# Optimization experiments

Measured on AMD Instinct MI355X. Metric: run time of the kernel, lower is better.

## Reference

```python
import jax, jax.numpy as jnp
import numpy as np

N = 100000
E = 1600000
EMB = 64
IN = 64
HID = 64
HEADS = 3
NEG_SLOPE = 0.2            # PyG GATConv default LeakyReLU slope
RRELU_SLOPE = (1.0 / 8.0 + 1.0 / 3.0) / 2.0  # torch.rrelu eval-mode slope


def setup_inputs() -> dict:
    key = jax.random.key(0)
    ks = jax.random.split(key, 16)
    d_in = IN + EMB
    inp = {
        "z": jax.random.normal(ks[0], (N, EMB), jnp.float32),
        "x": jax.random.normal(ks[1], (N, IN), jnp.float32),
        "edge_index": jax.random.randint(ks[2], (2, E), 0, N, jnp.int32),
        # gat1: (in+emb) -> hidden, 3 heads, concat=False
        "W1": jax.random.normal(ks[3], (d_in, HEADS * HID), jnp.float32) / np.sqrt(d_in),
        "att_src1": jax.random.normal(ks[4], (HEADS, HID), jnp.float32) / np.sqrt(HID),
        "att_dst1": jax.random.normal(ks[5], (HEADS, HID), jnp.float32) / np.sqrt(HID),
        "bias1": jnp.zeros((HID,), jnp.float32),
        # gat2: hidden -> hidden, 3 heads, concat=True
        "W2": jax.random.normal(ks[6], (HID, HEADS * HID), jnp.float32) / np.sqrt(HID),
        "att_src2": jax.random.normal(ks[7], (HEADS, HID), jnp.float32) / np.sqrt(HID),
        "att_dst2": jax.random.normal(ks[8], (HEADS, HID), jnp.float32) / np.sqrt(HID),
        "bias2": jnp.zeros((HEADS * HID,), jnp.float32),
        # final linear hidden*3 -> 1 (with bias)
        "lin_w": jax.random.normal(ks[9], (HEADS * HID, 1), jnp.float32) / np.sqrt(HEADS * HID),
        "lin_b": jnp.zeros((1,), jnp.float32),
    }
    return inp


def rrelu_eval(x):
    return jnp.where(x >= 0, x, x * RRELU_SLOPE)


def gat_conv(x, src, dst, W, a_src, a_dst, bias, concat):
    """PyG GATConv (shared src/dst projection, self-loops already appended)."""
    n = x.shape[0]
    H, C = a_src.shape
    xl = (x @ W).reshape(n, H, C)                       # [N, H, C]
    s = jnp.einsum('nhc,hc->nh', xl, a_src)             # alpha_src per node
    d = jnp.einsum('nhc,hc->nh', xl, a_dst)             # alpha_dst per node
    alpha = jax.nn.leaky_relu(s[src] + d[dst], NEG_SLOPE)  # [E', H]
    amax = jax.ops.segment_max(alpha, dst, num_segments=n)
    ex = jnp.exp(alpha - amax[dst])
    denom = jax.ops.segment_sum(ex, dst, num_segments=n)
    w = ex / (denom[dst] + 1e-16)                       # segment softmax
    out = jax.ops.segment_sum(xl[src] * w[:, :, None], dst, num_segments=n)  # [N,H,C]
    out = out.reshape(n, H * C) if concat else out.mean(axis=1)
    return out + bias


def reference(z, x, edge_index, W1, att_src1, att_dst1, bias1,
              W2, att_src2, att_dst2, bias2, lin_w, lin_b):
    n = x.shape[0]
    loops = jnp.arange(n, dtype=edge_index.dtype)
    src = jnp.concatenate([edge_index[0], loops])       # add self-loops (PyG default)
    dst = jnp.concatenate([edge_index[1], loops])
    h = jnp.concatenate([z, x], axis=1)
    h = rrelu_eval(gat_conv(h, src, dst, W1, att_src1, att_dst1, bias1, concat=False))
    h = rrelu_eval(gat_conv(h, src, dst, W2, att_src2, att_dst2, bias2, concat=True))
    return h @ lin_w + lin_b
```

## Files before the change

### kernel.cpp

```cpp
#include <hip/hip_runtime.h>
#include <cstdint>
#include <cstddef>

#define NEG_SLOPE 0.2f
#define RRELU_SLOPE 0.22916666666666666f

#define BSHIFT 6
#define BCAP 1536
#define MAXNB 1600

typedef _Float16 half4 __attribute__((ext_vector_type(4)));
typedef _Float16 half8 __attribute__((ext_vector_type(8)));
typedef float f32x4 __attribute__((ext_vector_type(4)));

__device__ __forceinline__ float wave_sum64(float v) {
#pragma unroll
  for (int o = 32; o > 0; o >>= 1) v += __shfl_xor(v, o, 64);
  return v;
}

__global__ __launch_bounds__(256) void bucketA(const int* __restrict__ src,
                                               const int* __restrict__ dst, int E, int NB,
                                               int* __restrict__ cursor,
                                               int* __restrict__ region) {
  __shared__ int hist[MAXNB];
  __shared__ int gbase[MAXNB];
  const int tid = threadIdx.x;
  const int chunk = (E + gridDim.x - 1) / gridDim.x;
  const int e0 = blockIdx.x * chunk;
  const int e1 = min(e0 + chunk, E);
  for (int b = tid; b < NB; b += 256) hist[b] = 0;
  __syncthreads();
  for (int i = e0 + tid; i < e1; i += 256) {
    atomicAdd(&hist[dst[i] >> BSHIFT], 1);
  }
  __syncthreads();
  for (int b = tid; b < NB; b += 256) {
    int c = hist[b];
    gbase[b] = (c > 0) ? atomicAdd(&cursor[b], c) : 0;
    hist[b] = 0;
  }
  __syncthreads();
  for (int i = e0 + tid; i < e1; i += 256) {
    int d = dst[i];
    int b = d >> BSHIFT;
    int idx = atomicAdd(&hist[b], 1) + gbase[b];
    if (idx < BCAP) region[b * BCAP + idx] = src[i] | ((d & 63) << 17);
  }
}

__global__ __launch_bounds__(256) void bucket_scan(const int* __restrict__ cursor, int NB,
                                                   int* __restrict__ colbase) {
  __shared__ int lds[256];
  const int tid = threadIdx.x;
  const int K = (NB + 255) / 256;
  int vals[8];
  int s = 0;
#pragma unroll
  for (int j = 0; j < 8; j++) {
    int b = tid * K + j;
    int v = (j < K && b < NB) ? (min(cursor[b], BCAP) + 64) : 0;
    vals[j] = v;
    s += v;
  }
  lds[tid] = s;
  __syncthreads();
  for (int o = 1; o < 256; o <<= 1) {
    int t = (tid >= o) ? lds[tid - o] : 0;
    __syncthreads();
    lds[tid] += t;
    __syncthreads();
  }
  int off = (tid > 0) ? lds[tid - 1] : 0;
#pragma unroll
  for (int j = 0; j < 8; j++) {
    int b = tid * K + j;
    if (j < K && b < NB) colbase[b] = off;
    off += vals[j];
  }
}

__global__ __launch_bounds__(256) void bucketB(const int* __restrict__ region,
                                               const int* __restrict__ cursor,
                                               const int* __restrict__ colbase, int NB,
                                               int* __restrict__ rp, int* __restrict__ col) {
  __shared__ int lcnt[64];
  __shared__ int loff[64];
  const int b = blockIdx.x;
  const int tid = threadIdx.x;
  const int cnt = min(cursor[b], BCAP);
  const int base = colbase[b];
  if (tid < 64) lcnt[tid] = 0;
  __syncthreads();
  const int* reg = region + (size_t)b * BCAP;
  for (int i = tid; i < cnt; i += 256) {
    atomicAdd(&lcnt[reg[i] >> 17], 1);
  }
  __syncthreads();
  if (tid < 64) {
    int v = lcnt[tid] + 1;
    int inc = v;
#pragma unroll
    for (int o = 1; o < 64; o <<= 1) {
      int t = __shfl_up(inc, o, 64);
      if (tid >= o) inc += t;
    }
    int excl = inc - v;
    loff[tid] = excl;
    int n = (b << BSHIFT) + tid;
    rp[n] = base + excl;
    col[base + excl] = n;
    lcnt[tid] = 1;
  }
  __syncthreads();
  for (int i = tid; i < cnt; i += 256) {
    int r = reg[i];
    int ld = r >> 17;
    int idx = atomicAdd(&lcnt[ld], 1);
    col[base + loff[ld] + idx] = r & 0x1FFFF;
  }
}

#define APAD 72
#define BTPAD 72

template <int KC>
__global__ __launch_bounds__(256, 4) void gemm_sd_kernel(
    const float* __restrict__ A0, const float* __restrict__ A1,
    const float* __restrict__ W, const float* __restrict__ asrc,
    const float* __restrict__ adst, _Float16* __restrict__ xlh,
    float* __restrict__ sdS, float* __restrict__ sdD, int N) {
  __shared__ _Float16 A16[64 * APAD];
  __shared__ _Float16 Bt[192 * BTPAD];
  const int tid = threadIdx.x;
  const int w = tid >> 6;
  const int lane = tid & 63;
  const int m = lane & 15;
  const int q = lane >> 4;
  const int m0 = blockIdx.x * 64;

  f32x4 acc[12];
#pragma unroll
  for (int t = 0; t < 12; t++) acc[t] = (f32x4)(0.f);

  for (int kc = 0; kc < KC; kc++) {
    const float* __restrict__ Ab = (KC == 2 && kc == 1) ? A1 : A0;
    if (kc > 0) __syncthreads();
#pragma unroll
    for (int i = 0; i < 4; i++) {
      int f = tid + 256 * i;
      int row = f >> 4;
      int c4 = f & 15;
      int gr = m0 + row;
      gr = (gr < N) ? gr : (N - 1);
      float4 v = *(const float4*)(Ab + (size_t)gr * 64 + c4 * 4);
      half4 hv;
      hv.x = (_Float16)v.x; hv.y = (_Float16)v.y;
      hv.z = (_Float16)v.z; hv.w = (_Float16)v.w;
      *(half4*)&A16[row * APAD + c4 * 4] = hv;
    }
#pragma unroll
    for (int i = 0; i < 6; i++) {
      int f = tid + 256 * i;
      int kg = f / 192;
      int c = f % 192;
      half8 hv;
#pragma unroll
      for (int j = 0; j < 8; j++) {
        hv[j] = (_Float16)W[(size_t)(kc * 64 + kg * 8 + j) * 192 + c];
      }
      *(half8*)&Bt[c * BTPAD + kg * 8] = hv;
    }
    __syncthreads();

#pragma unroll
    for (int t = 0; t < 2; t++) {
      half8 af = *(const half8*)&A16[(w * 16 + m) * APAD + t * 32 + q * 8];
#pragma unroll
      for (int ct = 0; ct < 12; ct++) {
        half8 bf = *(const half8*)&Bt[(ct * 16 + m) * BTPAD + t * 32 + q * 8];
        acc[ct] = __builtin_amdgcn_mfma_f32_16x16x32_f16(af, bf, acc[ct], 0, 0, 0);
      }
    }
  }

  float avs[12], avd[12];
#pragma unroll
  for (int ct = 0; ct < 12; ct++) {
    avs[ct] = asrc[ct * 16 + m];
    avd[ct] = adst[ct * 16 + m];
  }
#pragma unroll
  for (int r = 0; r < 4; r++) {
    const int gr = m0 + w * 16 + q * 4 + r;
    const bool ok = gr < N;
    if (ok) {
#pragma unroll
      for (int ct = 0; ct < 12; ct++) {
        xlh[(size_t)gr * 192 + ct * 16 + m] = (_Float16)acc[ct][r];
      }
    }
#pragma unroll
    for (int h = 0; h < 3; h++) {
      float ps = acc[h * 4 + 0][r] * avs[h * 4 + 0] + acc[h * 4 + 1][r] * avs[h * 4 + 1] +
                 acc[h * 4 + 2][r] * avs[h * 4 + 2] + acc[h * 4 + 3][r] * avs[h * 4 + 3];
      float pd = acc[h * 4 + 0][r] * avd[h * 4 + 0] + acc[h * 4 + 1][r] * avd[h * 4 + 1] +
                 acc[h * 4 + 2][r] * avd[h * 4 + 2] + acc[h * 4 + 3][r] * avd[h * 4 + 3];
#pragma unroll
      for (int o = 1; o < 16; o <<= 1) {
        ps += __shfl_xor(ps, o, 64);
        pd += __shfl_xor(pd, o, 64);
      }
      if (ok && m == 0) {
        sdS[(size_t)gr * 4 + h] = ps;
        sdD[(size_t)gr * 4 + h] = pd;
      }
    }
  }
}

template <int D>
__device__ __forceinline__ void gather_fma_d(const _Float16* __restrict__ xlh,
                                             const float4* __restrict__ eb, int t, int par,
                                             unsigned laneoff, int h, float* acc) {
  half8 xv[D];
#pragma unroll
  for (int u = 0; u < D; u++) {
    float4 rec = eb[2 * (t + u) + par];
    unsigned off = (unsigned)__float_as_int(rec.x) * 384u + laneoff;
    xv[u] = *(const half8*)((const char*)xlh + off);
  }
#pragma unroll
  for (int u = 0; u < D; u++) {
    float4 rec = eb[2 * (t + u) + par];
    float w = (h == 0) ? rec.y : ((h == 1) ? rec.z : rec.w);
#pragma unroll
    for (int k = 0; k < 8; k++) acc[k] += (float)xv[u][k] * w;
  }
}

template <int MODE>
__global__ __launch_bounds__(256) void agg_kernel(
    const _Float16* __restrict__ xlh, const float4* __restrict__ sdS,
    const float4* __restrict__ sdD, const int* __restrict__ rp,
    const int* __restrict__ col, const float* __restrict__ bias,
    const float* __restrict__ lw, const float* __restrict__ lb,
    float* __restrict__ out, int N) {
  __shared__ float4 ebuf[4][64];
  const int lane = threadIdx.x & 63;
  const int wv = threadIdx.x >> 6;
  const int n = blockIdx.x * 4 + wv;
  if (n >= N) return;
  const int beg = rp[n], end = rp[n + 1];
  const float4 dd = sdD[n];
  const int s = lane & 31;
  const int h = (s < 24) ? (s >> 3) : 0;
  const int g = s & 7;
  const int par = lane >> 5;
  const unsigned laneoff = (unsigned)(h * 128 + g * 16);

  float l0 = 0.f, l1 = 0.f, l2 = 0.f;
  float acc[8];
#pragma unroll
  for (int k = 0; k < 8; k++) acc[k] = 0.f;

  for (int j0 = beg; j0 < end; j0 += 64) {
    const int cntc = min(64, end - j0);
    const bool valid = lane < cntc;
    int srcv = valid ? col[j0 + lane] : 0;
    float4 s4 = sdS[srcv];
    float t0 = s4.x + dd.x, t1 = s4.y + dd.y, t2 = s4.z + dd.z;
    t0 = (t0 < 0.f) ? t0 * NEG_SLOPE : t0;
    t1 = (t1 < 0.f) ? t1 * NEG_SLOPE : t1;
    t2 = (t2 < 0.f) ? t2 * NEG_SLOPE : t2;
    float e0 = valid ? __expf(t0) : 0.f;
    float e1 = valid ? __expf(t1) : 0.f;
    float e2 = valid ? __expf(t2) : 0.f;
    l0 += e0; l1 += e1; l2 += e2;
    ebuf[wv][lane] = make_float4(__int_as_float(srcv), e0, e1, e2);
    const float4* eb = ebuf[wv];
    const int steps = (cntc + 1) >> 1;
    int t = 0;
    for (; t + 7 <= steps; t += 7) {
      gather_fma_d<7>(xlh, eb, t, par, laneoff, h, acc);
    }
    if (t + 4 <= steps) {
      gather_fma_d<4>(xlh, eb, t, par, laneoff, h, acc);
      t += 4;
    }
    if (t + 2 <= steps) {
      gather_fma_d<2>(xlh, eb, t, par, laneoff, h, acc);
      t += 2;
    }
    if (t < steps) {
      gather_fma_d<1>(xlh, eb, t, par, laneoff, h, acc);
    }
  }

#pragma unroll
  for (int k = 0; k < 8; k++) acc[k] += __shfl_xor(acc[k], 32, 64);
  l0 = wave_sum64(l0);
  l1 = wave_sum64(l1);
  l2 = wave_sum64(l2);
  const float invl = 1.0f / (((h == 0) ? l0 : ((h == 1) ? l1 : l2)) + 1e-16f);
  float v[8];
#pragma unroll
  for (int k = 0; k < 8; k++) v[k] = acc[k] * invl;

  if (MODE == 1) {
    float m[8];
#pragma unroll
    for (int k = 0; k < 8; k++) {
      float a0 = __shfl(v[k], g, 64);
      float a1 = __shfl(v[k], g + 8, 64);
      float a2 = __shfl(v[k], g + 16, 64);
      m[k] = (a0 + a1 + a2) * (1.f / 3.f);
    }
    if (lane < 8) {
      float4 b0 = *(const float4*)(bias + g * 8);
      float4 b1 = *(const float4*)(bias + g * 8 + 4);
      float4 r0, r1;
      r0.x = m[0] + b0.x; r0.y = m[1] + b0.y; r0.z = m[2] + b0.z; r0.w = m[3] + b0.w;
      r1.x = m[4] + b1.x; r1.y = m[5] + b1.y; r1.z = m[6] + b1.z; r1.w = m[7] + b1.w;
      r0.x = (r0.x < 0.f) ? r0.x * RRELU_SLOPE : r0.x;
      r0.y = (r0.y < 0.f) ? r0.y * RRELU_SLOPE : r0.y;
      r0.z = (r0.z < 0.f) ? r0.z * RRELU_SLOPE : r0.z;
      r0.w = (r0.w < 0.f) ? r0.w * RRELU_SLOPE : r0.w;
      r1.x = (r1.x < 0.f) ? r1.x * RRELU_SLOPE : r1.x;
      r1.y = (r1.y < 0.f) ? r1.y * RRELU_SLOPE : r1.y;
      r1.z = (r1.z < 0.f) ? r1.z * RRELU_SLOPE : r1.z;
      r1.w = (r1.w < 0.f) ? r1.w * RRELU_SLOPE : r1.w;
      *(float4*)(out + (size_t)n * 64 + g * 8) = r0;
      *(float4*)(out + (size_t)n * 64 + g * 8 + 4) = r1;
    }
  } else {
    float part = 0.f;
    if (lane < 24) {
      const int c0 = h * 64 + g * 8;
      float4 b0 = *(const float4*)(bias + c0);
      float4 b1 = *(const float4*)(bias + c0 + 4);
      float4 w0 = *(const float4*)(lw + c0);
      float4 w1 = *(const float4*)(lw + c0 + 4);
      float r;
      r = v[0] + b0.x; r = (r < 0.f) ? r * RRELU_SLOPE : r; part += r * w0.x;
      r = v[1] + b0.y; r = (r < 0.f) ? r * RRELU_SLOPE : r; part += r * w0.y;
      r = v[2] + b0.z; r = (r < 0.f) ? r * RRELU_SLOPE : r; part += r * w0.z;
      r = v[3] + b0.w; r = (r < 0.f) ? r * RRELU_SLOPE : r; part += r * w0.w;
      r = v[4] + b1.x; r = (r < 0.f) ? r * RRELU_SLOPE : r; part += r * w1.x;
      r = v[5] + b1.y; r = (r < 0.f) ? r * RRELU_SLOPE : r; part += r * w1.y;
      r = v[6] + b1.z; r = (r < 0.f) ? r * RRELU_SLOPE : r; part += r * w1.z;
      r = v[7] + b1.w; r = (r < 0.f) ? r * RRELU_SLOPE : r; part += r * w1.w;
    }
    part = wave_sum64(part);
    if (lane == 0) out[n] = part + lb[0];
  }
}

extern "C" void kernel_launch(void* const* d_in, const int* in_sizes, int n_in,
                              void* d_out, int out_size, void* d_ws, size_t ws_size,
                              hipStream_t stream) {
  const float* z   = (const float*)d_in[0];
  const float* x   = (const float*)d_in[1];
  const int*   ei  = (const int*)d_in[2];
  const float* W1  = (const float*)d_in[3];
  const float* as1 = (const float*)d_in[4];
  const float* ad1 = (const float*)d_in[5];
  const float* b1  = (const float*)d_in[6];
  const float* W2  = (const float*)d_in[7];
  const float* as2 = (const float*)d_in[8];
  const float* ad2 = (const float*)d_in[9];
  const float* b2  = (const float*)d_in[10];
  const float* lw  = (const float*)d_in[11];
  const float* lb  = (const float*)d_in[12];
  float* out = (float*)d_out;

  const int N = in_sizes[0] / 64;
  const int E = in_sizes[2] / 2;
  const int* srcA = ei;
  const int* dstA = ei + E;
  const int NB = (N + 63) >> BSHIFT;

  char* ws = (char*)d_ws;
  size_t off = 0;
  auto alloc = [&](size_t bytes) -> void* {
    void* p = ws + off;
    off = (off + bytes + 255) & ~(size_t)255;
    return p;
  };
  _Float16* xlh = (_Float16*)alloc((size_t)N * 192 * 2);
  float* h1  = (float*)alloc((size_t)N * 64 * 4);
  float* sdS = (float*)alloc((size_t)N * 4 * 4);
  float* sdD = (float*)alloc((size_t)N * 4 * 4);
  int* region  = (int*)alloc((size_t)NB * BCAP * 4);
  int* cursor  = (int*)alloc((size_t)NB * 4);
  int* colbase = (int*)alloc((size_t)NB * 4);
  int* rp      = (int*)alloc(((size_t)NB * 64 + 1) * 4);
  int* col     = (int*)alloc(((size_t)E + (size_t)NB * 64) * 4);
  if (off > ws_size) return;

  hipMemsetAsync(cursor, 0, (size_t)NB * 4, stream);
  bucketA<<<128, 256, 0, stream>>>(srcA, dstA, E, NB, cursor, region);
  bucket_scan<<<1, 256, 0, stream>>>(cursor, NB, colbase);
  bucketB<<<NB, 256, 0, stream>>>(region, cursor, colbase, NB, rp, col);

  dim3 gg((N + 63) / 64);
  gemm_sd_kernel<2><<<gg, 256, 0, stream>>>(z, x, W1, as1, ad1, xlh, sdS, sdD, N);
  agg_kernel<1><<<(N + 3) / 4, 256, 0, stream>>>(xlh, (const float4*)sdS, (const float4*)sdD,
                                                 rp, col, b1, nullptr, nullptr, h1, N);
  gemm_sd_kernel<1><<<gg, 256, 0, stream>>>(h1, nullptr, W2, as2, ad2, xlh, sdS, sdD, N);
  agg_kernel<2><<<(N + 3) / 4, 256, 0, stream>>>(xlh, (const float4*)sdS, (const float4*)sdD,
                                                 rp, col, b2, lw, lb, out, N);
}
```

Before: 427.5 us.

## Fuse edge bucketing into first GEMM launch, pre-transpose weights, persistent aggregation

Edge bucketing (bucketA) now runs inside the same launch as the first projection GEMM, with distinct block ranges doing each job so the two independent stages overlap and one launch disappears. The weights are converted to transposed fp16 once by a small kernel, so GEMM blocks load them as vector half8 reads instead of strided scalar float loads with conversion. The aggregation kernels become grid-stride loops over a capped grid, which cuts block scheduling overhead. The trade-offs are an extra small launch for the weight conversion, dynamic shared memory sized to the larger GEMM footprint, and the bucketing blocks possibly serialising behind GEMM blocks.

```diff
diff --git a/kernel.cpp b/kernel.cpp
--- a/kernel.cpp
+++ b/kernel.cpp
@@ -19,15 +19,27 @@
   return v;
 }
 
-__global__ __launch_bounds__(256) void bucketA(const int* __restrict__ src,
-                                               const int* __restrict__ dst, int E, int NB,
-                                               int* __restrict__ cursor,
-                                               int* __restrict__ region) {
-  __shared__ int hist[MAXNB];
-  __shared__ int gbase[MAXNB];
+__global__ __launch_bounds__(256) void wcvt_kernel(const float* __restrict__ W1,
+                                                   const float* __restrict__ W2,
+                                                   _Float16* __restrict__ Wt1,
+                                                   _Float16* __restrict__ Wt2) {
+  const int c = blockIdx.x;
+  for (int k = threadIdx.x; k < 128; k += 256)
+    Wt1[(size_t)c * 128 + k] = (_Float16)W1[(size_t)k * 192 + c];
+  for (int k = threadIdx.x; k < 64; k += 256)
+    Wt2[(size_t)c * 64 + k] = (_Float16)W2[(size_t)k * 192 + c];
+}
+
+__device__ __forceinline__ void bucketA_body(char* smem, int bid, int nblk,
+                                             const int* __restrict__ src,
+                                             const int* __restrict__ dst, int E, int NB,
+                                             int* __restrict__ cursor,
+                                             int* __restrict__ region) {
+  int* hist = (int*)smem;
+  int* gbase = hist + MAXNB;
   const int tid = threadIdx.x;
-  const int chunk = (E + gridDim.x - 1) / gridDim.x;
-  const int e0 = blockIdx.x * chunk;
+  const int chunk = (E + nblk - 1) / nblk;
+  const int e0 = bid * chunk;
   const int e1 = min(e0 + chunk, E);
   for (int b = tid; b < NB; b += 256) hist[b] = 0;
   __syncthreads();
@@ -123,21 +135,23 @@
 
 #define APAD 72
 #define BTPAD 72
+#define GEMM_LDS (64 * APAD * 2 + 192 * BTPAD * 2)
 
 template <int KC>
-__global__ __launch_bounds__(256, 4) void gemm_sd_kernel(
+__device__ __forceinline__ void gemm_body(char* smem, int bid,
     const float* __restrict__ A0, const float* __restrict__ A1,
-    const float* __restrict__ W, const float* __restrict__ asrc,
+    const _Float16* __restrict__ Wt, const float* __restrict__ asrc,
     const float* __restrict__ adst, _Float16* __restrict__ xlh,
     float* __restrict__ sdS, float* __restrict__ sdD, int N) {
-  __shared__ _Float16 A16[64 * APAD];
-  __shared__ _Float16 Bt[192 * BTPAD];
+  _Float16* A16 = (_Float16*)smem;
+  _Float16* Bt = A16 + 64 * APAD;
   const int tid = threadIdx.x;
   const int w = tid >> 6;
   const int lane = tid & 63;
   const int m = lane & 15;
   const int q = lane >> 4;
-  const int m0 = blockIdx.x * 64;
+  const int m0 = bid * 64;
+  const int KW = KC * 64;
 
   f32x4 acc[12];
 #pragma unroll
@@ -164,11 +178,7 @@
       int f = tid + 256 * i;
       int kg = f / 192;
       int c = f % 192;
-      half8 hv;
-#pragma unroll
-      for (int j = 0; j < 8; j++) {
-        hv[j] = (_Float16)W[(size_t)(kc * 64 + kg * 8 + j) * 192 + c];
-      }
+      half8 hv = *(const half8*)&Wt[(size_t)c * KW + kc * 64 + kg * 8];
       *(half8*)&Bt[c * BTPAD + kg * 8] = hv;
     }
     __syncthreads();
@@ -216,6 +226,22 @@
         sdD[(size_t)gr * 4 + h] = pd;
       }
     }
+  }
+}
+
+template <int KC>
+__global__ __launch_bounds__(256, 4) void gemm_bucketA_fused(
+    const float* __restrict__ A0, const float* __restrict__ A1,
+    const _Float16* __restrict__ Wt, const float* __restrict__ asrc,
+    const float* __restrict__ adst, _Float16* __restrict__ xlh,
+    float* __restrict__ sdS, float* __restrict__ sdD, int N,
+    const int* __restrict__ src, const int* __restrict__ dst, int E, int NB,
+    int* __restrict__ cursor, int* __restrict__ region, int NBA) {
+  extern __shared__ char smem[];
+  if ((int)blockIdx.x < NBA) {
+    bucketA_body(smem, blockIdx.x, NBA, src, dst, E, NB, cursor, region);
+  } else {
+    gemm_body<KC>(smem, blockIdx.x - NBA, A0, A1, Wt, asrc, adst, xlh, sdS, sdD, N);
   }
 }
 
@@ -249,110 +275,112 @@
   __shared__ float4 ebuf[4][64];
   const int lane = threadIdx.x & 63;
   const int wv = threadIdx.x >> 6;
-  const int n = blockIdx.x * 4 + wv;
-  if (n >= N) return;
-  const int beg = rp[n], end = rp[n + 1];
-  const float4 dd = sdD[n];
   const int s = lane & 31;
   const int h = (s < 24) ? (s >> 3) : 0;
   const int g = s & 7;
   const int par = lane >> 5;
   const unsigned laneoff = (unsigned)(h * 128 + g * 16);
-
-  float l0 = 0.f, l1 = 0.f, l2 = 0.f;
-  float acc[8];
-#pragma unroll
-  for (int k = 0; k < 8; k++) acc[k] = 0.f;
-
-  for (int j0 = beg; j0 < end; j0 += 64) {
-    const int cntc = min(64, end - j0);
-    const bool valid = lane < cntc;
-    int srcv = valid ? col[j0 + lane] : 0;
-    float4 s4 = sdS[srcv];
-    float t0 = s4.x + dd.x, t1 = s4.y + dd.y, t2 = s4.z + dd.z;
-    t0 = (t0 < 0.f) ? t0 * NEG_SLOPE : t0;
-    t1 = (t1 < 0.f) ? t1 * NEG_SLOPE : t1;
-    t2 = (t2 < 0.f) ? t2 * NEG_SLOPE : t2;
-    float e0 = valid ? __expf(t0) : 0.f;
-    float e1 = valid ? __expf(t1) : 0.f;
-    float e2 = valid ? __expf(t2) : 0.f;
-    l0 += e0; l1 += e1; l2 += e2;
-    ebuf[wv][lane] = make_float4(__int_as_float(srcv), e0, e1, e2);
-    const float4* eb = ebuf[wv];
-    const int steps = (cntc + 1) >> 1;
-    int t = 0;
-    for (; t + 7 <= steps; t += 7) {
-      gather_fma_d<7>(xlh, eb, t, par, laneoff, h, acc);
-    }
-    if (t + 4 <= steps) {
-      gather_fma_d<4>(xlh, eb, t, par, laneoff, h, acc);
-      t += 4;
-    }
-    if (t + 2 <= steps) {
-      gather_fma_d<2>(xlh, eb, t, par, laneoff, h, acc);
-      t += 2;
-    }
-    if (t < steps) {
-      gather_fma_d<1>(xlh, eb, t, par, laneoff, h, acc);
-    }
-  }
-
-#pragma unroll
-  for (int k = 0; k < 8; k++) acc[k] += __shfl_xor(acc[k], 32, 64);
-  l0 = wave_sum64(l0);
-  l1 = wave_sum64(l1);
-  l2 = wave_sum64(l2);
-  const float invl = 1.0f / (((h == 0) ? l0 : ((h == 1) ? l1 : l2)) + 1e-16f);
-  float v[8];
-#pragma unroll
-  for (int k = 0; k < 8; k++) v[k] = acc[k] * invl;
-
-  if (MODE == 1) {
-    float m[8];
-#pragma unroll
-    for (int k = 0; k < 8; k++) {
-      float a0 = __shfl(v[k], g, 64);
-      float a1 = __shfl(v[k], g + 8, 64);
-      float a2 = __shfl(v[k], g + 16, 64);
-      m[k] = (a0 + a1 + a2) * (1.f / 3.f);
-    }
-    if (lane < 8) {
-      float4 b0 = *(const float4*)(bias + g * 8);
-      float4 b1 = *(const float4*)(bias + g * 8 + 4);
-      float4 r0, r1;
-      r0.x = m[0] + b0.x; r0.y = m[1] + b0.y; r0.z = m[2] + b0.z; r0.w = m[3] + b0.w;
-      r1.x = m[4] + b1.x; r1.y = m[5] + b1.y; r1.z = m[6] + b1.z; r1.w = m[7] + b1.w;
-      r0.x = (r0.x < 0.f) ? r0.x * RRELU_SLOPE : r0.x;
-      r0.y = (r0.y < 0.f) ? r0.y * RRELU_SLOPE : r0.y;
-      r0.z = (r0.z < 0.f) ? r0.z * RRELU_SLOPE : r0.z;
-      r0.w = (r0.w < 0.f) ? r0.w * RRELU_SLOPE : r0.w;
-      r1.x = (r1.x < 0.f) ? r1.x * RRELU_SLOPE : r1.x;
-      r1.y = (r1.y < 0.f) ? r1.y * RRELU_SLOPE : r1.y;
-      r1.z = (r1.z < 0.f) ? r1.z * RRELU_SLOPE : r1.z;
-      r1.w = (r1.w < 0.f) ? r1.w * RRELU_SLOPE : r1.w;
-      *(float4*)(out + (size_t)n * 64 + g * 8) = r0;
-      *(float4*)(out + (size_t)n * 64 + g * 8 + 4) = r1;
-    }
-  } else {
-    float part = 0.f;
-    if (lane < 24) {
-      const int c0 = h * 64 + g * 8;
-      float4 b0 = *(const float4*)(bias + c0);
-      float4 b1 = *(const float4*)(bias + c0 + 4);
-      float4 w0 = *(const float4*)(lw + c0);
-      float4 w1 = *(const float4*)(lw + c0 + 4);
-      float r;
-      r = v[0] + b0.x; r = (r < 0.f) ? r * RRELU_SLOPE : r; part += r * w0.x;
-      r = v[1] + b0.y; r = (r < 0.f) ? r * RRELU_SLOPE : r; part += r * w0.y;
-      r = v[2] + b0.z; r = (r < 0.f) ? r * RRELU_SLOPE : r; part += r * w0.z;
-      r = v[3] + b0.w; r = (r < 0.f) ? r * RRELU_SLOPE : r; part += r * w0.w;
-      r = v[4] + b1.x; r = (r < 0.f) ? r * RRELU_SLOPE : r; part += r * w1.x;
-      r = v[5] + b1.y; r = (r < 0.f) ? r * RRELU_SLOPE : r; part += r * w1.y;
-      r = v[6] + b1.z; r = (r < 0.f) ? r * RRELU_SLOPE : r; part += r * w1.z;
-      r = v[7] + b1.w; r = (r < 0.f) ? r * RRELU_SLOPE : r; part += r * w1.w;
-    }
-    part = wave_sum64(part);
-    if (lane == 0) out[n] = part + lb[0];
+  const int stride = gridDim.x * 4;
+
+  for (int n = blockIdx.x * 4 + wv; n < N; n += stride) {
+    const int beg = rp[n], end = rp[n + 1];
+    const float4 dd = sdD[n];
+
+    float l0 = 0.f, l1 = 0.f, l2 = 0.f;
+    float acc[8];
+#pragma unroll
+    for (int k = 0; k < 8; k++) acc[k] = 0.f;
+
+    for (int j0 = beg; j0 < end; j0 += 64) {
+      const int cntc = min(64, end - j0);
+      const bool valid = lane < cntc;
+      int srcv = valid ? col[j0 + lane] : 0;
+      float4 s4 = sdS[srcv];
+      float t0 = s4.x + dd.x, t1 = s4.y + dd.y, t2 = s4.z + dd.z;
+      t0 = (t0 < 0.f) ? t0 * NEG_SLOPE : t0;
+      t1 = (t1 < 0.f) ? t1 * NEG_SLOPE : t1;
+      t2 = (t2 < 0.f) ? t2 * NEG_SLOPE : t2;
+      float e0 = valid ? __expf(t0) : 0.f;
+      float e1 = valid ? __expf(t1) : 0.f;
+      float e2 = valid ? __expf(t2) : 0.f;
+      l0 += e0; l1 += e1; l2 += e2;
+      ebuf[wv][lane] = make_float4(__int_as_float(srcv), e0, e1, e2);
+      const float4* eb = ebuf[wv];
+      const int steps = (cntc + 1) >> 1;
+      int t = 0;
+      for (; t + 7 <= steps; t += 7) {
+        gather_fma_d<7>(xlh, eb, t, par, laneoff, h, acc);
+      }
+      if (t + 4 <= steps) {
+        gather_fma_d<4>(xlh, eb, t, par, laneoff, h, acc);
+        t += 4;
+      }
+      if (t + 2 <= steps) {
+        gather_fma_d<2>(xlh, eb, t, par, laneoff, h, acc);
+        t += 2;
+      }
+      if (t < steps) {
+        gather_fma_d<1>(xlh, eb, t, par, laneoff, h, acc);
+      }
+    }
+
+#pragma unroll
+    for (int k = 0; k < 8; k++) acc[k] += __shfl_xor(acc[k], 32, 64);
+    l0 = wave_sum64(l0);
+    l1 = wave_sum64(l1);
+    l2 = wave_sum64(l2);
+    const float invl = 1.0f / (((h == 0) ? l0 : ((h == 1) ? l1 : l2)) + 1e-16f);
+    float v[8];
+#pragma unroll
+    for (int k = 0; k < 8; k++) v[k] = acc[k] * invl;
+
+    if (MODE == 1) {
+      float m[8];
+#pragma unroll
+      for (int k = 0; k < 8; k++) {
+        float a0 = __shfl(v[k], g, 64);
+        float a1 = __shfl(v[k], g + 8, 64);
+        float a2 = __shfl(v[k], g + 16, 64);
+        m[k] = (a0 + a1 + a2) * (1.f / 3.f);
+      }
+      if (lane < 8) {
+        float4 b0 = *(const float4*)(bias + g * 8);
+        float4 b1 = *(const float4*)(bias + g * 8 + 4);
+        float4 r0, r1;
+        r0.x = m[0] + b0.x; r0.y = m[1] + b0.y; r0.z = m[2] + b0.z; r0.w = m[3] + b0.w;
+        r1.x = m[4] + b1.x; r1.y = m[5] + b1.y; r1.z = m[6] + b1.z; r1.w = m[7] + b1.w;
+        r0.x = (r0.x < 0.f) ? r0.x * RRELU_SLOPE : r0.x;
+        r0.y = (r0.y < 0.f) ? r0.y * RRELU_SLOPE : r0.y;
+        r0.z = (r0.z < 0.f) ? r0.z * RRELU_SLOPE : r0.z;
+        r0.w = (r0.w < 0.f) ? r0.w * RRELU_SLOPE : r0.w;
+        r1.x = (r1.x < 0.f) ? r1.x * RRELU_SLOPE : r1.x;
+        r1.y = (r1.y < 0.f) ? r1.y * RRELU_SLOPE : r1.y;
+        r1.z = (r1.z < 0.f) ? r1.z * RRELU_SLOPE : r1.z;
+        r1.w = (r1.w < 0.f) ? r1.w * RRELU_SLOPE : r1.w;
+        *(float4*)(out + (size_t)n * 64 + g * 8) = r0;
+        *(float4*)(out + (size_t)n * 64 + g * 8 + 4) = r1;
+      }
+    } else {
+      float part = 0.f;
+      if (lane < 24) {
+        const int c0 = h * 64 + g * 8;
+        float4 b0 = *(const float4*)(bias + c0);
+        float4 b1 = *(const float4*)(bias + c0 + 4);
+        float4 w0 = *(const float4*)(lw + c0);
+        float4 w1 = *(const float4*)(lw + c0 + 4);
+        float r;
+        r = v[0] + b0.x; r = (r < 0.f) ? r * RRELU_SLOPE : r; part += r * w0.x;
+        r = v[1] + b0.y; r = (r < 0.f) ? r * RRELU_SLOPE : r; part += r * w0.y;
+        r = v[2] + b0.z; r = (r < 0.f) ? r * RRELU_SLOPE : r; part += r * w0.z;
+        r = v[3] + b0.w; r = (r < 0.f) ? r * RRELU_SLOPE : r; part += r * w0.w;
+        r = v[4] + b1.x; r = (r < 0.f) ? r * RRELU_SLOPE : r; part += r * w1.x;
+        r = v[5] + b1.y; r = (r < 0.f) ? r * RRELU_SLOPE : r; part += r * w1.y;
+        r = v[6] + b1.z; r = (r < 0.f) ? r * RRELU_SLOPE : r; part += r * w1.z;
+        r = v[7] + b1.w; r = (r < 0.f) ? r * RRELU_SLOPE : r; part += r * w1.w;
+      }
+      part = wave_sum64(part);
+      if (lane == 0) out[n] = part + lb[0];
+    }
   }
 }
 
@@ -379,6 +407,7 @@
   const int* srcA = ei;
   const int* dstA = ei + E;
   const int NB = (N + 63) >> BSHIFT;
+  const int NBA = 128;
 
   char* ws = (char*)d_ws;
   size_t off = 0;
@@ -391,6 +420,8 @@
   float* h1  = (float*)alloc((size_t)N * 64 * 4);
   float* sdS = (float*)alloc((size_t)N * 4 * 4);
   float* sdD = (float*)alloc((size_t)N * 4 * 4);
+  _Float16* Wt1 = (_Float16*)alloc((size_t)192 * 128 * 2);
+  _Float16* Wt2 = (_Float16*)alloc((size_t)192 * 64 * 2);
   int* region  = (int*)alloc((size_t)NB * BCAP * 4);
   int* cursor  = (int*)alloc((size_t)NB * 4);
   int* colbase = (int*)alloc((size_t)NB * 4);
@@ -399,15 +430,19 @@
   if (off > ws_size) return;
 
   hipMemsetAsync(cursor, 0, (size_t)NB * 4, stream);
-  bucketA<<<128, 256, 0, stream>>>(srcA, dstA, E, NB, cursor, region);
+  wcvt_kernel<<<192, 256, 0, stream>>>(W1, W2, Wt1, Wt2);
+
+  const int gg = (N + 63) / 64;
+  const int aggGrid = min((N + 3) / 4, 2048);
+  gemm_bucketA_fused<2><<<NBA + gg, 256, GEMM_LDS, stream>>>(
+      z, x, Wt1, as1, ad1, xlh, sdS, sdD, N, srcA, dstA, E, NB, cursor, region, NBA);
   bucket_scan<<<1, 256, 0, stream>>>(cursor, NB, colbase);
   bucketB<<<NB, 256, 0, stream>>>(region, cursor, colbase, NB, rp, col);
 
-  dim3 gg((N + 63) / 64);
-  gemm_sd_kernel<2><<<gg, 256, 0, stream>>>(z, x, W1, as1, ad1, xlh, sdS, sdD, N);
-  agg_kernel<1><<<(N + 3) / 4, 256, 0, stream>>>(xlh, (const float4*)sdS, (const float4*)sdD,
-                                                 rp, col, b1, nullptr, nullptr, h1, N);
-  gemm_sd_kernel<1><<<gg, 256, 0, stream>>>(h1, nullptr, W2, as2, ad2, xlh, sdS, sdD, N);
-  agg_kernel<2><<<(N + 3) / 4, 256, 0, stream>>>(xlh, (const float4*)sdS, (const float4*)sdD,
-                                                 rp, col, b2, lw, lb, out, N);
-}
+  agg_kernel<1><<<aggGrid, 256, 0, stream>>>(xlh, (const float4*)sdS, (const float4*)sdD,
+                                             rp, col, b1, nullptr, nullptr, h1, N);
+  gemm_bucketA_fused<1><<<gg, 256, GEMM_LDS, stream>>>(
+      h1, nullptr, Wt2, as2, ad2, xlh, sdS, sdD, N, nullptr, nullptr, 0, NB, nullptr, nullptr, 0);
+  agg_kernel<2><<<aggGrid, 256, 0, stream>>>(xlh, (const float4*)sdS, (const float4*)sdD,
+                                             rp, col, b2, lw, lb, out, N);
+}
```

Result: slower. 451.8 us (+5.7%).
